# Performance work log

Hardware: AMD Instinct MI355X
Metric: run time of the kernel (lower is better)

The kernel has to match this reference:

```python
import jax, jax.numpy as jnp
import numpy as np

E = 8        # num_experts
C = 1024     # n_emb
H = 4096     # n_emb * ff_mult
B, T = 4, 1024


def setup_inputs() -> dict:
    key = jax.random.key(0)
    k_x, k_g, k_1, k_2, k_3 = jax.random.split(key, 5)
    scale = 0.02
    return {
        "x": jax.random.normal(k_x, (B, T, C), dtype=jnp.float32),
        "Wg": jax.random.normal(k_g, (E, C), dtype=jnp.float32) * scale,   # gate: Linear(C, E), weight [E, C]
        "W1": jax.random.normal(k_1, (E, C, H), dtype=jnp.float32) * scale,  # per-expert w1 (transposed for einsum)
        "W2": jax.random.normal(k_2, (E, H, C), dtype=jnp.float32) * scale,  # per-expert w2
        "W3": jax.random.normal(k_3, (E, C, H), dtype=jnp.float32) * scale,  # per-expert w3
        "top_k": 2,
    }


def reference(x, Wg, W1, W2, W3, top_k):
    Bd, Td, Cd = x.shape
    xf = x.reshape(-1, Cd)                                   # [N, C]
    N = xf.shape[0]
    logits = jnp.einsum('nc,ec->ne', xf, Wg)                 # router logits [N, E]
    probs = jax.nn.softmax(logits.astype(jnp.float32), axis=-1)
    w, sel = jax.lax.top_k(probs, top_k)                     # [N, k]
    w = w / w.sum(axis=-1, keepdims=True)                    # renormalize over selected
    # combine weight per (token, expert): sum of normalized topk weights routed to e
    cw = jnp.zeros((N, E), jnp.float32).at[jnp.arange(N)[:, None], sel].add(w)
    # dense grouped SwiGLU over all experts; combine weights zero out unselected experts
    h1 = jnp.einsum('nc,ech->neh', xf, W1)                   # [N, E, H]
    g = jax.nn.silu(h1) * jnp.einsum('nc,ech->neh', xf, W3)  # [N, E, H]
    out = jnp.einsum('neh,ehc,ne->nc', g, W2, cw.astype(x.dtype))
    return out.reshape(Bd, Td, Cd)
```

## Files before the change

kernel.cpp:

```cpp
#include <hip/hip_runtime.h>
#include <hip/hip_bf16.h>

#define E_     8
#define C_     1024
#define H_     4096
#define N_TOK  4096
#define TOPK   2
#define NSLOT  (N_TOK*TOPK)
#define SPAD   (NSLOT+256)

#define LPAD 40

typedef __attribute__((ext_vector_type(4))) float f32x4;
typedef __attribute__((ext_vector_type(8))) short short8;

__device__ __forceinline__ unsigned short f2bf(float f) {
    return __builtin_bit_cast(unsigned short, __float2bfloat16(f));
}

__device__ __forceinline__ void gload16(const void* g, const void* l) {
    __builtin_amdgcn_global_load_lds(
        (const __attribute__((address_space(1))) unsigned int*)g,
        (__attribute__((address_space(3))) unsigned int*)l, 16, 0, 0);
}

#define WAITVM_(n) asm volatile("s_waitcnt vmcnt(" #n ")" ::: "memory")
#define WAITVM(n) WAITVM_(n)
#define SWZ(r) ((((r)&3) ^ (((r)>>2)&3)))

__global__ void router_kernel(const float* __restrict__ x, const float* __restrict__ Wg,
                              int* __restrict__ sel, float* __restrict__ wts) {
    int wave = (blockIdx.x * blockDim.x + threadIdx.x) >> 6;
    int lane = threadIdx.x & 63;
    if (wave >= N_TOK) return;
    const float* xr = x + (size_t)wave * C_;
    float acc[E_];
#pragma unroll
    for (int e = 0; e < E_; ++e) acc[e] = 0.f;
    for (int c = lane; c < C_; c += 64) {
        float xv = xr[c];
#pragma unroll
        for (int e = 0; e < E_; ++e) acc[e] += xv * Wg[e * C_ + c];
    }
#pragma unroll
    for (int e = 0; e < E_; ++e) {
#pragma unroll
        for (int off = 32; off > 0; off >>= 1) acc[e] += __shfl_xor(acc[e], off);
    }
    if (lane == 0) {
        float mx = acc[0];
#pragma unroll
        for (int e = 1; e < E_; ++e) mx = fmaxf(mx, acc[e]);
        float p[E_]; float s = 0.f;
#pragma unroll
        for (int e = 0; e < E_; ++e) { p[e] = __expf(acc[e] - mx); s += p[e]; }
        float inv = 1.f / s;
#pragma unroll
        for (int e = 0; e < E_; ++e) p[e] *= inv;
        int b0 = 0; float v0 = p[0];
#pragma unroll
        for (int e = 1; e < E_; ++e) if (p[e] > v0) { v0 = p[e]; b0 = e; }
        int b1 = -1; float v1 = -1.f;
#pragma unroll
        for (int e = 0; e < E_; ++e) { if (e != b0 && p[e] > v1) { v1 = p[e]; b1 = e; } }
        float isum = 1.f / (v0 + v1);
        sel[wave*2]   = b0; sel[wave*2+1] = b1;
        wts[wave*2]   = v0 * isum; wts[wave*2+1] = v1 * isum;
    }
}

__global__ void assign_kernel(const int* __restrict__ sel, const float* __restrict__ wts,
                              int* __restrict__ counts, int* __restrict__ offsets,
                              int* __restrict__ pos_of_slot, int* __restrict__ token_of,
                              float* __restrict__ slotw) {
    __shared__ int cnt[256][E_];
    __shared__ int offs[E_];
    int t = threadIdx.x;
    const int PER = NSLOT / 256;
    int base = t * PER;
    int loc[E_];
#pragma unroll
    for (int e = 0; e < E_; ++e) loc[e] = 0;
    for (int i = 0; i < PER; ++i) loc[sel[base + i]]++;
#pragma unroll
    for (int e = 0; e < E_; ++e) cnt[t][e] = loc[e];
    __syncthreads();
    if (t < E_) {
        int run = 0;
        for (int i = 0; i < 256; ++i) { int c = cnt[i][t]; cnt[i][t] = run; run += c; }
        counts[t] = run;
    }
    __syncthreads();
    if (t == 0) {
        int s = 0;
        for (int e = 0; e < E_; ++e) { offs[e] = s; offsets[e] = s; s += counts[e]; }
    }
    __syncthreads();
    int run[E_];
#pragma unroll
    for (int e = 0; e < E_; ++e) run[e] = offs[e] + cnt[t][e];
    for (int i = 0; i < PER; ++i) {
        int s = base + i;
        int e = sel[s];
        int p = run[e]++;
        pos_of_slot[s] = p;
        token_of[p] = s >> 1;
        slotw[p] = wts[s];
    }
}

__global__ void copy_kernel(const float* __restrict__ x, const int* __restrict__ pos_of_slot,
                            unsigned short* __restrict__ Xg) {
    int slot = blockIdx.x * 4 + (threadIdx.x >> 6);
    int lane = threadIdx.x & 63;
    int pos = pos_of_slot[slot];
    int n = slot >> 1;
    const float* xr = x + (size_t)n * C_;
    unsigned short* dst = Xg + (size_t)pos * C_;
#pragma unroll
    for (int i = 0; i < 4; ++i) {
        int c0 = i * 256 + lane * 4;
        float4 v = *(const float4*)(xr + c0);
        ushort4 b;
        b.x = f2bf(v.x); b.y = f2bf(v.y); b.z = f2bf(v.z); b.w = f2bf(v.w);
        *(ushort4*)(dst + c0) = b;
    }
}

__global__ void wconv_kernel(const float* __restrict__ src, unsigned short* __restrict__ dst,
                             int R, int Cc) {
    int e = blockIdx.z;
    int c0 = blockIdx.x * 64;
    int r0 = blockIdx.y * 64;
    const float* s = src + (size_t)e * R * Cc;
    unsigned short* d = dst + (size_t)e * R * Cc;
    __shared__ unsigned short t_[64][72];
    int t = threadIdx.x;
    int tr = t >> 4, tc4 = (t & 15) * 4;
#pragma unroll
    for (int i = 0; i < 4; ++i) {
        int r = tr + i * 16;
        float4 v = *(const float4*)(s + (size_t)(r0 + r) * Cc + c0 + tc4);
        t_[r][tc4+0] = f2bf(v.x); t_[r][tc4+1] = f2bf(v.y);
        t_[r][tc4+2] = f2bf(v.z); t_[r][tc4+3] = f2bf(v.w);
    }
    __syncthreads();
    int oc = t >> 2, seg = (t & 3) * 16;
    short8 w0, w1;
#pragma unroll
    for (int j = 0; j < 8; ++j) {
        w0[j] = (short)t_[seg + j][oc];
        w1[j] = (short)t_[seg + 8 + j][oc];
    }
    unsigned short* dp = d + (size_t)(c0 + oc) * R + r0 + seg;
    *(short8*)dp = w0;
    *(short8*)(dp + 8) = w1;
}


#define G1_NH (C_/32)

__global__ __launch_bounds__(512, 2) void gemm1_ring(
        const unsigned short* __restrict__ Xg, const unsigned short* __restrict__ W1t,
        const unsigned short* __restrict__ W3t, unsigned short* __restrict__ G,
        const int* __restrict__ counts, const int* __restrict__ offsets) {
    int ct = blockIdx.x;
    int rslot = blockIdx.y;
    int e = rslot >> 5, rt = rslot & 31;
    int ne = counts[e];
    if (rt * 256 >= ne) return;
    int row0 = offsets[e] + rt * 256;
    int n0 = ct * 128;

    extern __shared__ char lds[];
    char* As  = lds;
    char* B1s = lds + 65536;
    char* B3s = lds + 98304;

    int tid = threadIdx.x, lane = tid & 63, wid = tid >> 6;
    int wm = wid >> 1, wn = wid & 1;
    int fr = lane & 15, q = lane >> 4;
    int srow = lane >> 2, pchk = lane & 3;

    const unsigned short* Ap  = Xg + (size_t)row0 * C_;
    const unsigned short* B1p = W1t + ((size_t)e * H_ + n0) * C_;
    const unsigned short* B3p = W3t + ((size_t)e * H_ + n0) * C_;

    f32x4 acc1[4][4], acc3[4][4];
#pragma unroll
    for (int m = 0; m < 4; ++m)
#pragma unroll
        for (int n = 0; n < 4; ++n) {
            acc1[m][n] = (f32x4){0.f,0.f,0.f,0.f};
            acc3[m][n] = (f32x4){0.f,0.f,0.f,0.f};
        }

    auto STAGE = [&](int hs, int slot) {
        int k0 = hs * 32;
#pragma unroll
        for (int r = 0; r < 2; ++r) {
            int row = r*128 + wid*16 + srow;
            int sc = pchk ^ SWZ(row);
            gload16(Ap + (size_t)row * C_ + k0 + sc*8,
                    As + slot*16384 + (r*128 + wid*16)*64);
        }
        {
            int row = wid*16 + srow;
            int sc = pchk ^ SWZ(row);
            gload16(B1p + (size_t)row * C_ + k0 + sc*8, B1s + slot*8192 + wid*1024);
            gload16(B3p + (size_t)row * C_ + k0 + sc*8, B3s + slot*8192 + wid*1024);
        }
    };

    STAGE(0, 0); STAGE(1, 1); STAGE(2, 2);
    WAITVM(8);
    __builtin_amdgcn_s_barrier();

    for (int h = 0; h < G1_NH; ++h) {
        int slot = h & 3;
        short8 a[4], b1[4], b3[4];
#pragma unroll
        for (int m = 0; m < 4; ++m) {
            int row = wm*64 + m*16 + fr;
            a[m] = *(const short8*)(As + slot*16384 + row*64 + ((q ^ SWZ(row)) << 4));
        }
#pragma unroll
        for (int n = 0; n < 4; ++n) {
            int row = wn*64 + n*16 + fr;
            int so = row*64 + ((q ^ SWZ(row)) << 4);
            b1[n] = *(const short8*)(B1s + slot*8192 + so);
            b3[n] = *(const short8*)(B3s + slot*8192 + so);
        }
        int hs = (h + 3 < G1_NH) ? h + 3 : G1_NH - 1;
        STAGE(hs, (h + 3) & 3);
        WAITVM(8);
        __builtin_amdgcn_sched_barrier(0);
        __builtin_amdgcn_s_setprio(1);
#pragma unroll
        for (int m = 0; m < 4; ++m)
#pragma unroll
            for (int n = 0; n < 4; ++n) {
                acc1[m][n] = __builtin_amdgcn_mfma_f32_16x16x32_bf16(a[m], b1[n], acc1[m][n], 0, 0, 0);
                acc3[m][n] = __builtin_amdgcn_mfma_f32_16x16x32_bf16(a[m], b3[n], acc3[m][n], 0, 0, 0);
            }
        __builtin_amdgcn_s_setprio(0);
        __builtin_amdgcn_s_barrier();
    }
    WAITVM(0);

#pragma unroll
    for (int m = 0; m < 4; ++m)
#pragma unroll
        for (int rg = 0; rg < 4; ++rg) {
            int row = wm*64 + m*16 + q*4 + rg;
            if (rt * 256 + row < ne) {
                size_t gbase = (size_t)(row0 + row) * H_ + n0 + wn*64;
#pragma unroll
                for (int n = 0; n < 4; ++n) {
                    float h1 = acc1[m][n][rg];
                    float h3 = acc3[m][n][rg];
                    float g = h1 * h3 / (1.f + __expf(-h1));
                    G[gbase + n*16 + fr] = f2bf(g);
                }
            }
        }
}

#define G2_NH (H_/32)

__global__ __launch_bounds__(512, 2) void gemm2_ring(
        const unsigned short* __restrict__ G, const unsigned short* __restrict__ W2t,
        float* __restrict__ out, const int* __restrict__ counts,
        const int* __restrict__ offsets, const int* __restrict__ token_of,
        const float* __restrict__ slotw) {
    int ct = blockIdx.x;
    int rslot = blockIdx.y;
    int e = rslot >> 5, rt = rslot & 31;
    int ne = counts[e];
    if (rt * 256 >= ne) return;
    int row0 = offsets[e] + rt * 256;
    int n0 = ct * 128;

    extern __shared__ char lds[];
    char* As = lds;
    char* Bs = lds + 65536;

    int tid = threadIdx.x, lane = tid & 63, wid = tid >> 6;
    int wm = wid >> 1, wn = wid & 1;
    int fr = lane & 15, q = lane >> 4;
    int srow = lane >> 2, pchk = lane & 3;

    const unsigned short* Ap = G + (size_t)row0 * H_;
    const unsigned short* Bp = W2t + ((size_t)e * C_ + n0) * H_;

    f32x4 acc[4][4];
#pragma unroll
    for (int m = 0; m < 4; ++m)
#pragma unroll
        for (int n = 0; n < 4; ++n) acc[m][n] = (f32x4){0.f,0.f,0.f,0.f};

    auto STAGE = [&](int hs, int slot) {
        int k0 = hs * 32;
#pragma unroll
        for (int r = 0; r < 2; ++r) {
            int row = r*128 + wid*16 + srow;
            int sc = pchk ^ SWZ(row);
            gload16(Ap + (size_t)row * H_ + k0 + sc*8,
                    As + slot*16384 + (r*128 + wid*16)*64);
        }
        {
            int row = wid*16 + srow;
            int sc = pchk ^ SWZ(row);
            gload16(Bp + (size_t)row * H_ + k0 + sc*8, Bs + slot*8192 + wid*1024);
        }
    };

    STAGE(0, 0); STAGE(1, 1); STAGE(2, 2);
    WAITVM(6);
    __builtin_amdgcn_s_barrier();

    for (int h = 0; h < G2_NH; ++h) {
        int slot = h & 3;
        short8 a[4], b[4];
#pragma unroll
        for (int m = 0; m < 4; ++m) {
            int row = wm*64 + m*16 + fr;
            a[m] = *(const short8*)(As + slot*16384 + row*64 + ((q ^ SWZ(row)) << 4));
        }
#pragma unroll
        for (int n = 0; n < 4; ++n) {
            int row = wn*64 + n*16 + fr;
            b[n] = *(const short8*)(Bs + slot*8192 + row*64 + ((q ^ SWZ(row)) << 4));
        }
        int hs = (h + 3 < G2_NH) ? h + 3 : G2_NH - 1;
        STAGE(hs, (h + 3) & 3);
        WAITVM(6);
        __builtin_amdgcn_sched_barrier(0);
        __builtin_amdgcn_s_setprio(1);
#pragma unroll
        for (int m = 0; m < 4; ++m)
#pragma unroll
            for (int n = 0; n < 4; ++n)
                acc[m][n] = __builtin_amdgcn_mfma_f32_16x16x32_bf16(a[m], b[n], acc[m][n], 0, 0, 0);
        __builtin_amdgcn_s_setprio(0);
        __builtin_amdgcn_s_barrier();
    }
    WAITVM(0);

#pragma unroll
    for (int m = 0; m < 4; ++m)
#pragma unroll
        for (int rg = 0; rg < 4; ++rg) {
            int row = wm*64 + m*16 + q*4 + rg;
            if (rt * 256 + row < ne) {
                int grow = row0 + row;
                int tok = token_of[grow];
                float w = slotw[grow];
                float* orow = out + (size_t)tok * C_ + n0 + wn*64;
#pragma unroll
                for (int n = 0; n < 4; ++n)
                    atomicAdd(orow + n*16 + fr, acc[m][n][rg] * w);
            }
        }
}

#define BM 128
#define BN 128
#define BK 32
__global__ __launch_bounds__(256, 2) void gemm1_slow(
        const unsigned short* __restrict__ Xg, const float* __restrict__ W1,
        const float* __restrict__ W3, unsigned short* __restrict__ G,
        const int* __restrict__ counts, const int* __restrict__ offsets) {
    int ct = blockIdx.x;
    int rslot = blockIdx.y;
    int e = rslot >> 5, rt = rslot & 31;
    int ne = counts[e];
    if (rt * BM >= ne) return;
    int row0 = offsets[e] + rt * BM;
    int n0 = ct * BN;

    __shared__ unsigned short As[BM][LPAD];
    __shared__ unsigned short B1s[BN][LPAD];
    __shared__ unsigned short B3s[BN][LPAD];

    int tid = threadIdx.x;
    int lane = tid & 63, wid = tid >> 6;
    int wr = (wid >> 1) * 64, wc = (wid & 1) * 64;

    f32x4 acc1[4][4], acc3[4][4];
#pragma unroll
    for (int m = 0; m < 4; ++m)
#pragma unroll
        for (int n = 0; n < 4; ++n) {
            acc1[m][n] = (f32x4){0.f,0.f,0.f,0.f};
            acc3[m][n] = (f32x4){0.f,0.f,0.f,0.f};
        }

    const float* B1p = W1 + (size_t)e * C_ * H_ + n0;
    const float* B3p = W3 + (size_t)e * C_ * H_ + n0;
    int chunk = tid & 3, rr = tid >> 2;
    int kq = tid >> 5, n4 = tid & 31;

    for (int k0 = 0; k0 < C_; k0 += BK) {
        __syncthreads();
#pragma unroll
        for (int h = 0; h < 2; ++h) {
            int row = rr + h * 64;
            uint4 v = *(const uint4*)(Xg + (size_t)(row0 + row) * C_ + k0 + chunk * 8);
            *(uint4*)&As[row][chunk * 8] = v;
        }
        {
            float4 r0 = *(const float4*)(B1p + (size_t)(k0 + kq*4 + 0) * H_ + n4*4);
            float4 r1 = *(const float4*)(B1p + (size_t)(k0 + kq*4 + 1) * H_ + n4*4);
            float4 r2 = *(const float4*)(B1p + (size_t)(k0 + kq*4 + 2) * H_ + n4*4);
            float4 r3 = *(const float4*)(B1p + (size_t)(k0 + kq*4 + 3) * H_ + n4*4);
            ushort4 w0 = {f2bf(r0.x), f2bf(r1.x), f2bf(r2.x), f2bf(r3.x)};
            ushort4 w1 = {f2bf(r0.y), f2bf(r1.y), f2bf(r2.y), f2bf(r3.y)};
            ushort4 w2 = {f2bf(r0.z), f2bf(r1.z), f2bf(r2.z), f2bf(r3.z)};
            ushort4 w3 = {f2bf(r0.w), f2bf(r1.w), f2bf(r2.w), f2bf(r3.w)};
            *(ushort4*)&B1s[n4*4+0][kq*4] = w0;
            *(ushort4*)&B1s[n4*4+1][kq*4] = w1;
            *(ushort4*)&B1s[n4*4+2][kq*4] = w2;
            *(ushort4*)&B1s[n4*4+3][kq*4] = w3;
            r0 = *(const float4*)(B3p + (size_t)(k0 + kq*4 + 0) * H_ + n4*4);
            r1 = *(const float4*)(B3p + (size_t)(k0 + kq*4 + 1) * H_ + n4*4);
            r2 = *(const float4*)(B3p + (size_t)(k0 + kq*4 + 2) * H_ + n4*4);
            r3 = *(const float4*)(B3p + (size_t)(k0 + kq*4 + 3) * H_ + n4*4);
            w0 = (ushort4){f2bf(r0.x), f2bf(r1.x), f2bf(r2.x), f2bf(r3.x)};
            w1 = (ushort4){f2bf(r0.y), f2bf(r1.y), f2bf(r2.y), f2bf(r3.y)};
            w2 = (ushort4){f2bf(r0.z), f2bf(r1.z), f2bf(r2.z), f2bf(r3.z)};
            w3 = (ushort4){f2bf(r0.w), f2bf(r1.w), f2bf(r2.w), f2bf(r3.w)};
            *(ushort4*)&B3s[n4*4+0][kq*4] = w0;
            *(ushort4*)&B3s[n4*4+1][kq*4] = w1;
            *(ushort4*)&B3s[n4*4+2][kq*4] = w2;
            *(ushort4*)&B3s[n4*4+3][kq*4] = w3;
        }
        __syncthreads();
        int q = lane >> 4, fr = lane & 15;
        short8 a[4], b1[4], b3[4];
#pragma unroll
        for (int m = 0; m < 4; ++m) a[m] = *(const short8*)&As[wr + m*16 + fr][q*8];
#pragma unroll
        for (int n = 0; n < 4; ++n) {
            b1[n] = *(const short8*)&B1s[wc + n*16 + fr][q*8];
            b3[n] = *(const short8*)&B3s[wc + n*16 + fr][q*8];
        }
#pragma unroll
        for (int m = 0; m < 4; ++m)
#pragma unroll
            for (int n = 0; n < 4; ++n) {
                acc1[m][n] = __builtin_amdgcn_mfma_f32_16x16x32_bf16(a[m], b1[n], acc1[m][n], 0, 0, 0);
                acc3[m][n] = __builtin_amdgcn_mfma_f32_16x16x32_bf16(a[m], b3[n], acc3[m][n], 0, 0, 0);
            }
    }
    int q = lane >> 4, cfr = lane & 15;
#pragma unroll
    for (int m = 0; m < 4; ++m) {
#pragma unroll
        for (int rg = 0; rg < 4; ++rg) {
            int row = wr + m*16 + q*4 + rg;
            if (rt * BM + row < ne) {
                size_t gbase = (size_t)(row0 + row) * H_ + n0;
#pragma unroll
                for (int n = 0; n < 4; ++n) {
                    float h1 = acc1[m][n][rg];
                    float h3 = acc3[m][n][rg];
                    float g = h1 * h3 / (1.f + __expf(-h1));
                    G[gbase + wc + n*16 + cfr] = f2bf(g);
                }
            }
        }
    }
}

__global__ __launch_bounds__(256, 2) void gemm2_slow(
        const unsigned short* __restrict__ G, const float* __restrict__ W2,
        float* __restrict__ out, const int* __restrict__ counts,
        const int* __restrict__ offsets, const int* __restrict__ token_of,
        const float* __restrict__ slotw) {
    int ct = blockIdx.x;
    int rslot = blockIdx.y;
    int e = rslot >> 5, rt = rslot & 31;
    int ne = counts[e];
    if (rt * BM >= ne) return;
    int row0 = offsets[e] + rt * BM;
    int n0 = ct * BN;

    __shared__ unsigned short As[BM][LPAD];
    __shared__ unsigned short Bs[BN][LPAD];

    int tid = threadIdx.x;
    int lane = tid & 63, wid = tid >> 6;
    int wr = (wid >> 1) * 64, wc = (wid & 1) * 64;

    f32x4 acc[4][4];
#pragma unroll
    for (int m = 0; m < 4; ++m)
#pragma unroll
        for (int n = 0; n < 4; ++n) acc[m][n] = (f32x4){0.f,0.f,0.f,0.f};

    const float* Bp = W2 + (size_t)e * H_ * C_ + n0;
    int chunk = tid & 3, rr = tid >> 2;
    int kq = tid >> 5, n4 = tid & 31;

    for (int k0 = 0; k0 < H_; k0 += BK) {
        __syncthreads();
#pragma unroll
        for (int h = 0; h < 2; ++h) {
            int row = rr + h * 64;
            uint4 v = *(const uint4*)(G + (size_t)(row0 + row) * H_ + k0 + chunk * 8);
            *(uint4*)&As[row][chunk * 8] = v;
        }
        {
            float4 r0 = *(const float4*)(Bp + (size_t)(k0 + kq*4 + 0) * C_ + n4*4);
            float4 r1 = *(const float4*)(Bp + (size_t)(k0 + kq*4 + 1) * C_ + n4*4);
            float4 r2 = *(const float4*)(Bp + (size_t)(k0 + kq*4 + 2) * C_ + n4*4);
            float4 r3 = *(const float4*)(Bp + (size_t)(k0 + kq*4 + 3) * C_ + n4*4);
            ushort4 w0 = {f2bf(r0.x), f2bf(r1.x), f2bf(r2.x), f2bf(r3.x)};
            ushort4 w1 = {f2bf(r0.y), f2bf(r1.y), f2bf(r2.y), f2bf(r3.y)};
            ushort4 w2 = {f2bf(r0.z), f2bf(r1.z), f2bf(r2.z), f2bf(r3.z)};
            ushort4 w3 = {f2bf(r0.w), f2bf(r1.w), f2bf(r2.w), f2bf(r3.w)};
            *(ushort4*)&Bs[n4*4+0][kq*4] = w0;
            *(ushort4*)&Bs[n4*4+1][kq*4] = w1;
            *(ushort4*)&Bs[n4*4+2][kq*4] = w2;
            *(ushort4*)&Bs[n4*4+3][kq*4] = w3;
        }
        __syncthreads();
        int q = lane >> 4, fr = lane & 15;
        short8 a[4], b[4];
#pragma unroll
        for (int m = 0; m < 4; ++m) a[m] = *(const short8*)&As[wr + m*16 + fr][q*8];
#pragma unroll
        for (int n = 0; n < 4; ++n) b[n] = *(const short8*)&Bs[wc + n*16 + fr][q*8];
#pragma unroll
        for (int m = 0; m < 4; ++m)
#pragma unroll
            for (int n = 0; n < 4; ++n)
                acc[m][n] = __builtin_amdgcn_mfma_f32_16x16x32_bf16(a[m], b[n], acc[m][n], 0, 0, 0);
    }
    int q = lane >> 4, cfr = lane & 15;
#pragma unroll
    for (int m = 0; m < 4; ++m) {
#pragma unroll
        for (int rg = 0; rg < 4; ++rg) {
            int row = wr + m*16 + q*4 + rg;
            if (rt * BM + row < ne) {
                int grow = row0 + row;
                int tok = token_of[grow];
                float w = slotw[grow];
                float* orow = out + (size_t)tok * C_ + n0;
#pragma unroll
                for (int n = 0; n < 4; ++n)
                    atomicAdd(orow + wc + n*16 + cfr, acc[m][n][rg] * w);
            }
        }
    }
}

extern "C" void kernel_launch(void* const* d_in, const int* in_sizes, int n_in,
                              void* d_out, int out_size, void* d_ws, size_t ws_size,
                              hipStream_t stream) {
    const float* x  = (const float*)d_in[0];
    const float* Wg = (const float*)d_in[1];
    const float* W1 = (const float*)d_in[2];
    const float* W2 = (const float*)d_in[3];
    const float* W3 = (const float*)d_in[4];
    float* out = (float*)d_out;

    char* ws = (char*)d_ws;
    size_t o = 0;
    int*   sel      = (int*)(ws + o);  o += (size_t)NSLOT * 4;
    float* wts      = (float*)(ws + o); o += (size_t)NSLOT * 4;
    int*   pos      = (int*)(ws + o);  o += (size_t)NSLOT * 4;
    int*   token_of = (int*)(ws + o);  o += (size_t)NSLOT * 4;
    float* slotw    = (float*)(ws + o); o += (size_t)NSLOT * 4;
    int*   counts   = (int*)(ws + o);
    int*   offsets  = counts + E_;     o += 256;
    unsigned short* Xg = (unsigned short*)(ws + o); o += (size_t)SPAD * C_ * 2;
    unsigned short* G  = (unsigned short*)(ws + o); o += (size_t)SPAD * H_ * 2;
    size_t need_slow = o;
    unsigned short* W1t = (unsigned short*)(ws + o); o += (size_t)E_ * H_ * C_ * 2;
    unsigned short* W3t = (unsigned short*)(ws + o); o += (size_t)E_ * H_ * C_ * 2;
    unsigned short* W2t = W1t;
    size_t need_fast = o;

    hipMemsetAsync(d_out, 0, (size_t)out_size * sizeof(float), stream);
    if (ws_size < need_slow) return;

    router_kernel<<<N_TOK/4, 256, 0, stream>>>(x, Wg, sel, wts);
    assign_kernel<<<1, 256, 0, stream>>>(sel, wts, counts, offsets, pos, token_of, slotw);
    copy_kernel<<<NSLOT/4, 256, 0, stream>>>(x, pos, Xg);

    if (ws_size >= need_fast) {
        hipFuncSetAttribute((const void*)gemm1_ring, hipFuncAttributeMaxDynamicSharedMemorySize, 131072);
        hipFuncSetAttribute((const void*)gemm2_ring, hipFuncAttributeMaxDynamicSharedMemorySize, 98304);
        wconv_kernel<<<dim3(H_/64, C_/64, E_), 256, 0, stream>>>(W1, W1t, C_, H_);
        wconv_kernel<<<dim3(H_/64, C_/64, E_), 256, 0, stream>>>(W3, W3t, C_, H_);
        gemm1_ring<<<dim3(H_/128, E_*32), 512, 131072, stream>>>(Xg, W1t, W3t, G, counts, offsets);
        wconv_kernel<<<dim3(C_/64, H_/64, E_), 256, 0, stream>>>(W2, W2t, H_, C_);
        gemm2_ring<<<dim3(C_/128, E_*32), 512, 98304, stream>>>(G, W2t, out, counts, offsets, token_of, slotw);
    } else {
        gemm1_slow<<<dim3(H_/BN, E_*32), 256, 0, stream>>>(Xg, W1, W3, G, counts, offsets);
        gemm2_slow<<<dim3(C_/BN, E_*32), 256, 0, stream>>>(G, W2, out, counts, offsets, token_of, slotw);
    }
}
```

Baseline: 501.2 us.

## Use fragment-major LDS layout and split gate/up MFMA phases with extra barriers

Replaces the XOR-swizzled row-major LDS tile layout with a fragment-major layout: each lane loads 16 rows by 4 k-chunks and writes them so MFMA operand reads become contiguous 16-byte reads with no swizzle arithmetic. In the gate/up GEMM the main loop is split into two phases, W1 MFMAs then W3 MFMAs, with A staging and B staging interleaved between them and extra workgroup barriers. This is meant to cut LDS bank conflicts and address math and to overlap loads with compute more finely. The cost is extra barriers per iteration and fewer independent MFMAs per phase. Global loads now read 16 rows with strided addresses per wave, which may coalesce less well.

```diff
diff --git a/kernel.cpp b/kernel.cpp
--- a/kernel.cpp
+++ b/kernel.cpp
@@ -26,7 +26,6 @@
 
 #define WAITVM_(n) asm volatile("s_waitcnt vmcnt(" #n ")" ::: "memory")
 #define WAITVM(n) WAITVM_(n)
-#define SWZ(r) ((((r)&3) ^ (((r)>>2)&3)))
 
 __global__ void router_kernel(const float* __restrict__ x, const float* __restrict__ Wg,
                               int* __restrict__ sel, float* __restrict__ wts) {
@@ -180,7 +179,7 @@
     int tid = threadIdx.x, lane = tid & 63, wid = tid >> 6;
     int wm = wid >> 1, wn = wid & 1;
     int fr = lane & 15, q = lane >> 4;
-    int srow = lane >> 2, pchk = lane & 3;
+    int arow = lane & 15, akch = lane >> 4;
 
     const unsigned short* Ap  = Xg + (size_t)row0 * C_;
     const unsigned short* B1p = W1t + ((size_t)e * H_ + n0) * C_;
@@ -195,54 +194,64 @@
             acc3[m][n] = (f32x4){0.f,0.f,0.f,0.f};
         }
 
-    auto STAGE = [&](int hs, int slot) {
+    auto STAGE_A = [&](int hs, int slot) {
         int k0 = hs * 32;
 #pragma unroll
-        for (int r = 0; r < 2; ++r) {
-            int row = r*128 + wid*16 + srow;
-            int sc = pchk ^ SWZ(row);
-            gload16(Ap + (size_t)row * C_ + k0 + sc*8,
-                    As + slot*16384 + (r*128 + wid*16)*64);
-        }
-        {
-            int row = wid*16 + srow;
-            int sc = pchk ^ SWZ(row);
-            gload16(B1p + (size_t)row * C_ + k0 + sc*8, B1s + slot*8192 + wid*1024);
-            gload16(B3p + (size_t)row * C_ + k0 + sc*8, B3s + slot*8192 + wid*1024);
+        for (int j = 0; j < 2; ++j) {
+            int g = wid + j * 8;
+            gload16(Ap + (size_t)(g * 16 + arow) * C_ + k0 + akch * 8,
+                    As + slot * 16384 + g * 1024);
         }
     };
-
-    STAGE(0, 0); STAGE(1, 1); STAGE(2, 2);
+    auto STAGE_B = [&](int hs, int slot) {
+        int k0 = hs * 32;
+        gload16(B1p + (size_t)(wid * 16 + arow) * C_ + k0 + akch * 8,
+                B1s + slot * 8192 + wid * 1024);
+        gload16(B3p + (size_t)(wid * 16 + arow) * C_ + k0 + akch * 8,
+                B3s + slot * 8192 + wid * 1024);
+    };
+
+    STAGE_A(0, 0); STAGE_B(0, 0);
+    STAGE_A(1, 1); STAGE_B(1, 1);
+    STAGE_A(2, 2); STAGE_B(2, 2);
     WAITVM(8);
     __builtin_amdgcn_s_barrier();
 
     for (int h = 0; h < G1_NH; ++h) {
         int slot = h & 3;
+        int hs = (h + 3 < G1_NH) ? h + 3 : G1_NH - 1;
+        int wslot = (h + 3) & 3;
         short8 a[4], b1[4], b3[4];
 #pragma unroll
-        for (int m = 0; m < 4; ++m) {
-            int row = wm*64 + m*16 + fr;
-            a[m] = *(const short8*)(As + slot*16384 + row*64 + ((q ^ SWZ(row)) << 4));
-        }
-#pragma unroll
-        for (int n = 0; n < 4; ++n) {
-            int row = wn*64 + n*16 + fr;
-            int so = row*64 + ((q ^ SWZ(row)) << 4);
-            b1[n] = *(const short8*)(B1s + slot*8192 + so);
-            b3[n] = *(const short8*)(B3s + slot*8192 + so);
-        }
-        int hs = (h + 3 < G1_NH) ? h + 3 : G1_NH - 1;
-        STAGE(hs, (h + 3) & 3);
+        for (int m = 0; m < 4; ++m)
+            a[m] = *(const short8*)(As + slot * 16384 + (wm * 4 + m) * 1024 + q * 256 + fr * 16);
+#pragma unroll
+        for (int n = 0; n < 4; ++n)
+            b1[n] = *(const short8*)(B1s + slot * 8192 + (wn * 4 + n) * 1024 + q * 256 + fr * 16);
+        STAGE_A(hs, wslot);
+        __builtin_amdgcn_sched_barrier(0);
+        __builtin_amdgcn_s_barrier();
+        __builtin_amdgcn_s_setprio(1);
+#pragma unroll
+        for (int m = 0; m < 4; ++m)
+#pragma unroll
+            for (int n = 0; n < 4; ++n)
+                acc1[m][n] = __builtin_amdgcn_mfma_f32_16x16x32_bf16(a[m], b1[n], acc1[m][n], 0, 0, 0);
+        __builtin_amdgcn_s_setprio(0);
+        __builtin_amdgcn_s_barrier();
+#pragma unroll
+        for (int n = 0; n < 4; ++n)
+            b3[n] = *(const short8*)(B3s + slot * 8192 + (wn * 4 + n) * 1024 + q * 256 + fr * 16);
+        STAGE_B(hs, wslot);
         WAITVM(8);
         __builtin_amdgcn_sched_barrier(0);
+        __builtin_amdgcn_s_barrier();
         __builtin_amdgcn_s_setprio(1);
 #pragma unroll
         for (int m = 0; m < 4; ++m)
 #pragma unroll
-            for (int n = 0; n < 4; ++n) {
-                acc1[m][n] = __builtin_amdgcn_mfma_f32_16x16x32_bf16(a[m], b1[n], acc1[m][n], 0, 0, 0);
+            for (int n = 0; n < 4; ++n)
                 acc3[m][n] = __builtin_amdgcn_mfma_f32_16x16x32_bf16(a[m], b3[n], acc3[m][n], 0, 0, 0);
-            }
         __builtin_amdgcn_s_setprio(0);
         __builtin_amdgcn_s_barrier();
     }
@@ -288,7 +297,7 @@
     int tid = threadIdx.x, lane = tid & 63, wid = tid >> 6;
     int wm = wid >> 1, wn = wid & 1;
     int fr = lane & 15, q = lane >> 4;
-    int srow = lane >> 2, pchk = lane & 3;
+    int arow = lane & 15, akch = lane >> 4;
 
     const unsigned short* Ap = G + (size_t)row0 * H_;
     const unsigned short* Bp = W2t + ((size_t)e * C_ + n0) * H_;
@@ -302,17 +311,13 @@
     auto STAGE = [&](int hs, int slot) {
         int k0 = hs * 32;
 #pragma unroll
-        for (int r = 0; r < 2; ++r) {
-            int row = r*128 + wid*16 + srow;
-            int sc = pchk ^ SWZ(row);
-            gload16(Ap + (size_t)row * H_ + k0 + sc*8,
-                    As + slot*16384 + (r*128 + wid*16)*64);
-        }
-        {
-            int row = wid*16 + srow;
-            int sc = pchk ^ SWZ(row);
-            gload16(Bp + (size_t)row * H_ + k0 + sc*8, Bs + slot*8192 + wid*1024);
-        }
+        for (int j = 0; j < 2; ++j) {
+            int g = wid + j * 8;
+            gload16(Ap + (size_t)(g * 16 + arow) * H_ + k0 + akch * 8,
+                    As + slot * 16384 + g * 1024);
+        }
+        gload16(Bp + (size_t)(wid * 16 + arow) * H_ + k0 + akch * 8,
+                Bs + slot * 8192 + wid * 1024);
     };
 
     STAGE(0, 0); STAGE(1, 1); STAGE(2, 2);
@@ -321,21 +326,18 @@
 
     for (int h = 0; h < G2_NH; ++h) {
         int slot = h & 3;
+        int hs = (h + 3 < G2_NH) ? h + 3 : G2_NH - 1;
         short8 a[4], b[4];
 #pragma unroll
-        for (int m = 0; m < 4; ++m) {
-            int row = wm*64 + m*16 + fr;
-            a[m] = *(const short8*)(As + slot*16384 + row*64 + ((q ^ SWZ(row)) << 4));
-        }
-#pragma unroll
-        for (int n = 0; n < 4; ++n) {
-            int row = wn*64 + n*16 + fr;
-            b[n] = *(const short8*)(Bs + slot*8192 + row*64 + ((q ^ SWZ(row)) << 4));
-        }
-        int hs = (h + 3 < G2_NH) ? h + 3 : G2_NH - 1;
+        for (int m = 0; m < 4; ++m)
+            a[m] = *(const short8*)(As + slot * 16384 + (wm * 4 + m) * 1024 + q * 256 + fr * 16);
+#pragma unroll
+        for (int n = 0; n < 4; ++n)
+            b[n] = *(const short8*)(Bs + slot * 8192 + (wn * 4 + n) * 1024 + q * 256 + fr * 16);
         STAGE(hs, (h + 3) & 3);
         WAITVM(6);
         __builtin_amdgcn_sched_barrier(0);
+        __builtin_amdgcn_s_barrier();
         __builtin_amdgcn_s_setprio(1);
 #pragma unroll
         for (int m = 0; m < 4; ++m)
```

Result: slower. 590.4 us (+17.8%).

## Use 256x256 GEMM tiles with interleaved W1/W3 layout and split-K GEMM2

Applied to the files above, without the earlier changes.

The W1 and W3 weights are converted into one interleaved bf16 buffer, so GEMM1 runs a single 256x256 tile that yields paired h1/h3 columns for the SwiGLU epilogue. Both GEMMs switch from a 4-slot ring with K=32 steps to a double-buffered K=64 pipeline. It has four phases per step, issuing half-tile loads between barrier-separated MFMA groups and using an 8-row-group LDS layout. GEMM2 now uses 256-wide output tiles and a 4-way split of the H reduction across blocks, which raises parallelism and reuse but quadruples the atomic adds into the output. The larger tiles and more barriers per step may lower occupancy, and the layout drops the earlier XOR swizzle, which could introduce LDS bank conflicts.

```diff
diff --git a/kernel.cpp b/kernel.cpp
--- a/kernel.cpp
+++ b/kernel.cpp
@@ -26,7 +26,6 @@
 
 #define WAITVM_(n) asm volatile("s_waitcnt vmcnt(" #n ")" ::: "memory")
 #define WAITVM(n) WAITVM_(n)
-#define SWZ(r) ((((r)&3) ^ (((r)>>2)&3)))
 
 __global__ void router_kernel(const float* __restrict__ x, const float* __restrict__ Wg,
                               int* __restrict__ sel, float* __restrict__ wts) {
@@ -157,12 +156,44 @@
     *(short8*)(dp + 8) = w1;
 }
 
-
-#define G1_NH (C_/32)
-
-__global__ __launch_bounds__(512, 2) void gemm1_ring(
-        const unsigned short* __restrict__ Xg, const unsigned short* __restrict__ W1t,
-        const unsigned short* __restrict__ W3t, unsigned short* __restrict__ G,
+__global__ void wconv13_kernel(const float* __restrict__ src, unsigned short* __restrict__ dst,
+                               int is3) {
+    int e = blockIdx.z;
+    int c0 = blockIdx.x * 64;
+    int r0 = blockIdx.y * 64;
+    const float* s = src + (size_t)e * C_ * H_;
+    unsigned short* d = dst + (size_t)e * 8192 * C_;
+    __shared__ unsigned short t_[64][72];
+    int t = threadIdx.x;
+    int tr = t >> 4, tc4 = (t & 15) * 4;
+#pragma unroll
+    for (int i = 0; i < 4; ++i) {
+        int r = tr + i * 16;
+        float4 v = *(const float4*)(s + (size_t)(r0 + r) * H_ + c0 + tc4);
+        t_[r][tc4+0] = f2bf(v.x); t_[r][tc4+1] = f2bf(v.y);
+        t_[r][tc4+2] = f2bf(v.z); t_[r][tc4+3] = f2bf(v.w);
+    }
+    __syncthreads();
+    int oc = t >> 2, seg = (t & 3) * 16;
+    short8 w0, w1;
+#pragma unroll
+    for (int j = 0; j < 8; ++j) {
+        w0[j] = (short)t_[seg + j][oc];
+        w1[j] = (short)t_[seg + 8 + j][oc];
+    }
+    int h = c0 + oc;
+    int nI = ((h >> 4) << 5) + (h & 15) + is3 * 16;
+    unsigned short* dp = d + (size_t)nI * C_ + r0 + seg;
+    *(short8*)dp = w0;
+    *(short8*)(dp + 8) = w1;
+}
+
+
+#define LDSOFF(lr, kc) ((((lr) >> 3) << 10) + ((kc) << 7) + (((lr) & 7) << 4))
+
+__global__ __launch_bounds__(512, 2) void gemm1_256(
+        const unsigned short* __restrict__ Xg, const unsigned short* __restrict__ W13t,
+        unsigned short* __restrict__ G,
         const int* __restrict__ counts, const int* __restrict__ offsets) {
     int ct = blockIdx.x;
     int rslot = blockIdx.y;
@@ -170,196 +201,194 @@
     int ne = counts[e];
     if (rt * 256 >= ne) return;
     int row0 = offsets[e] + rt * 256;
-    int n0 = ct * 128;
 
     extern __shared__ char lds[];
-    char* As  = lds;
-    char* B1s = lds + 65536;
-    char* B3s = lds + 98304;
 
     int tid = threadIdx.x, lane = tid & 63, wid = tid >> 6;
-    int wm = wid >> 1, wn = wid & 1;
+    int wm = wid >> 2, wn = wid & 3;
     int fr = lane & 15, q = lane >> 4;
-    int srow = lane >> 2, pchk = lane & 3;
-
-    const unsigned short* Ap  = Xg + (size_t)row0 * C_;
-    const unsigned short* B1p = W1t + ((size_t)e * H_ + n0) * C_;
-    const unsigned short* B3p = W3t + ((size_t)e * H_ + n0) * C_;
-
-    f32x4 acc1[4][4], acc3[4][4];
-#pragma unroll
-    for (int m = 0; m < 4; ++m)
-#pragma unroll
-        for (int n = 0; n < 4; ++n) {
-            acc1[m][n] = (f32x4){0.f,0.f,0.f,0.f};
-            acc3[m][n] = (f32x4){0.f,0.f,0.f,0.f};
-        }
-
-    auto STAGE = [&](int hs, int slot) {
-        int k0 = hs * 32;
-#pragma unroll
-        for (int r = 0; r < 2; ++r) {
-            int row = r*128 + wid*16 + srow;
-            int sc = pchk ^ SWZ(row);
-            gload16(Ap + (size_t)row * C_ + k0 + sc*8,
-                    As + slot*16384 + (r*128 + wid*16)*64);
-        }
-        {
-            int row = wid*16 + srow;
-            int sc = pchk ^ SWZ(row);
-            gload16(B1p + (size_t)row * C_ + k0 + sc*8, B1s + slot*8192 + wid*1024);
-            gload16(B3p + (size_t)row * C_ + k0 + sc*8, B3s + slot*8192 + wid*1024);
+    int sr = lane & 7, sc = lane >> 3;
+
+    const unsigned short* Ap = Xg + (size_t)row0 * C_;
+    const unsigned short* Bp = W13t + ((size_t)e * 8192 + ct * 256) * C_;
+
+    f32x4 acc[8][4];
+#pragma unroll
+    for (int m = 0; m < 8; ++m)
+#pragma unroll
+        for (int n = 0; n < 4; ++n) acc[m][n] = (f32x4){0.f,0.f,0.f,0.f};
+
+    auto STAGE_A = [&](int ts, int half, int dd) {
+        int k0 = ts * 64;
+#pragma unroll
+        for (int j = 0; j < 2; ++j) {
+            int g = wid * 2 + j;
+            int row = half * 128 + g * 8 + sr;
+            gload16(Ap + (size_t)row * C_ + k0 + sc * 8,
+                    lds + dd * 65536 + half * 16384 + g * 1024);
         }
     };
-
-    STAGE(0, 0); STAGE(1, 1); STAGE(2, 2);
-    WAITVM(8);
-    __builtin_amdgcn_s_barrier();
-
-    for (int h = 0; h < G1_NH; ++h) {
-        int slot = h & 3;
-        short8 a[4], b1[4], b3[4];
-#pragma unroll
-        for (int m = 0; m < 4; ++m) {
-            int row = wm*64 + m*16 + fr;
-            a[m] = *(const short8*)(As + slot*16384 + row*64 + ((q ^ SWZ(row)) << 4));
-        }
-#pragma unroll
-        for (int n = 0; n < 4; ++n) {
-            int row = wn*64 + n*16 + fr;
-            int so = row*64 + ((q ^ SWZ(row)) << 4);
-            b1[n] = *(const short8*)(B1s + slot*8192 + so);
-            b3[n] = *(const short8*)(B3s + slot*8192 + so);
-        }
-        int hs = (h + 3 < G1_NH) ? h + 3 : G1_NH - 1;
-        STAGE(hs, (h + 3) & 3);
-        WAITVM(8);
-        __builtin_amdgcn_sched_barrier(0);
-        __builtin_amdgcn_s_setprio(1);
-#pragma unroll
-        for (int m = 0; m < 4; ++m)
-#pragma unroll
-            for (int n = 0; n < 4; ++n) {
-                acc1[m][n] = __builtin_amdgcn_mfma_f32_16x16x32_bf16(a[m], b1[n], acc1[m][n], 0, 0, 0);
-                acc3[m][n] = __builtin_amdgcn_mfma_f32_16x16x32_bf16(a[m], b3[n], acc3[m][n], 0, 0, 0);
-            }
-        __builtin_amdgcn_s_setprio(0);
-        __builtin_amdgcn_s_barrier();
+    auto STAGE_B = [&](int ts, int half, int dd) {
+        int k0 = ts * 64;
+#pragma unroll
+        for (int j = 0; j < 2; ++j) {
+            int g = wid * 2 + j;
+            int row = half * 128 + g * 8 + sr;
+            gload16(Bp + (size_t)row * C_ + k0 + sc * 8,
+                    lds + dd * 65536 + 32768 + half * 16384 + g * 1024);
+        }
+    };
+
+    STAGE_A(0, 0, 0); STAGE_A(0, 1, 0); STAGE_B(0, 0, 0); STAGE_B(0, 1, 0);
+
+    const int NT = C_ / 64;
+    short8 af[4], bf_[4];
+    for (int t = 0; t < NT; ++t) {
+        int d = t & 1, dn = d ^ 1;
+        int ts = (t + 1 < NT) ? t + 1 : t;
+        const char* Abase = lds + d * 65536 + wm * 16384;
+        const char* Bbase = lds + d * 65536 + 32768 + (wn >> 1) * 16384;
+
+#define G1_PH(STG, WN, KS, MH, RDB)                                                  \
+        __builtin_amdgcn_s_barrier();                                                \
+        STG;                                                                         \
+        WAITVM(WN);                                                                  \
+        __builtin_amdgcn_s_barrier();                                                \
+        __builtin_amdgcn_sched_barrier(0);                                           \
+        {                                                                            \
+            int kc = (KS) * 4 + q;                                                   \
+            _Pragma("unroll")                                                        \
+            for (int m = 0; m < 4; ++m) {                                            \
+                int lr = ((MH) * 4 + m) * 16 + fr;                                   \
+                af[m] = *(const short8*)(Abase + LDSOFF(lr, kc));                    \
+            }                                                                        \
+            if (RDB) {                                                               \
+                _Pragma("unroll")                                                    \
+                for (int n = 0; n < 4; ++n) {                                        \
+                    int lrb = (wn & 1) * 64 + n * 16 + fr;                           \
+                    bf_[n] = *(const short8*)(Bbase + LDSOFF(lrb, kc));              \
+                }                                                                    \
+            }                                                                        \
+            __builtin_amdgcn_s_setprio(1);                                           \
+            _Pragma("unroll")                                                        \
+            for (int m = 0; m < 4; ++m)                                              \
+                _Pragma("unroll")                                                    \
+                for (int n = 0; n < 4; ++n)                                          \
+                    acc[(MH)*4 + m][n] = __builtin_amdgcn_mfma_f32_16x16x32_bf16(    \
+                        af[m], bf_[n], acc[(MH)*4 + m][n], 0, 0, 0);                 \
+            __builtin_amdgcn_s_setprio(0);                                           \
+        }
+
+        G1_PH(STAGE_A(ts, 0, dn), 2, 0, 0, 1)
+        G1_PH(STAGE_A(ts, 1, dn), 4, 0, 1, 0)
+        G1_PH(STAGE_B(ts, 0, dn), 6, 1, 0, 1)
+        G1_PH(STAGE_B(ts, 1, dn), 8, 1, 1, 0)
     }
     WAITVM(0);
 
 #pragma unroll
-    for (int m = 0; m < 4; ++m)
+    for (int m = 0; m < 8; ++m)
 #pragma unroll
         for (int rg = 0; rg < 4; ++rg) {
-            int row = wm*64 + m*16 + q*4 + rg;
+            int row = wm * 128 + m * 16 + q * 4 + rg;
             if (rt * 256 + row < ne) {
-                size_t gbase = (size_t)(row0 + row) * H_ + n0 + wn*64;
-#pragma unroll
-                for (int n = 0; n < 4; ++n) {
-                    float h1 = acc1[m][n][rg];
-                    float h3 = acc3[m][n][rg];
+                size_t gbase = (size_t)(row0 + row) * H_;
+#pragma unroll
+                for (int pi = 0; pi < 2; ++pi) {
+                    float h1 = acc[m][2 * pi][rg];
+                    float h3 = acc[m][2 * pi + 1][rg];
                     float g = h1 * h3 / (1.f + __expf(-h1));
-                    G[gbase + n*16 + fr] = f2bf(g);
+                    int h = (ct * 8 + wn * 2 + pi) * 16 + fr;
+                    G[gbase + h] = f2bf(g);
                 }
             }
         }
 }
 
-#define G2_NH (H_/32)
-
-__global__ __launch_bounds__(512, 2) void gemm2_ring(
+__global__ __launch_bounds__(512, 2) void gemm2_256(
         const unsigned short* __restrict__ G, const unsigned short* __restrict__ W2t,
         float* __restrict__ out, const int* __restrict__ counts,
         const int* __restrict__ offsets, const int* __restrict__ token_of,
         const float* __restrict__ slotw) {
-    int ct = blockIdx.x;
-    int rslot = blockIdx.y;
-    int e = rslot >> 5, rt = rslot & 31;
+    int b = blockIdx.x;
+    int e = b & 7;
+    int j = b >> 3;
+    int ksp = j & 3;
+    int ct = (j >> 2) & 3;
+    int rt = j >> 4;
     int ne = counts[e];
     if (rt * 256 >= ne) return;
     int row0 = offsets[e] + rt * 256;
-    int n0 = ct * 128;
+    int n0 = ct * 256;
+    int kbase = ksp * (H_ / 4);
 
     extern __shared__ char lds[];
-    char* As = lds;
-    char* Bs = lds + 65536;
 
     int tid = threadIdx.x, lane = tid & 63, wid = tid >> 6;
-    int wm = wid >> 1, wn = wid & 1;
+    int wm = wid >> 2, wn = wid & 3;
     int fr = lane & 15, q = lane >> 4;
-    int srow = lane >> 2, pchk = lane & 3;
-
-    const unsigned short* Ap = G + (size_t)row0 * H_;
-    const unsigned short* Bp = W2t + ((size_t)e * C_ + n0) * H_;
-
-    f32x4 acc[4][4];
-#pragma unroll
-    for (int m = 0; m < 4; ++m)
+    int sr = lane & 7, sc = lane >> 3;
+
+    const unsigned short* Ap = G + (size_t)row0 * H_ + kbase;
+    const unsigned short* Bp = W2t + ((size_t)e * C_ + n0) * H_ + kbase;
+
+    f32x4 acc[8][4];
+#pragma unroll
+    for (int m = 0; m < 8; ++m)
 #pragma unroll
         for (int n = 0; n < 4; ++n) acc[m][n] = (f32x4){0.f,0.f,0.f,0.f};
 
-    auto STAGE = [&](int hs, int slot) {
-        int k0 = hs * 32;
-#pragma unroll
-        for (int r = 0; r < 2; ++r) {
-            int row = r*128 + wid*16 + srow;
-            int sc = pchk ^ SWZ(row);
-            gload16(Ap + (size_t)row * H_ + k0 + sc*8,
-                    As + slot*16384 + (r*128 + wid*16)*64);
-        }
-        {
-            int row = wid*16 + srow;
-            int sc = pchk ^ SWZ(row);
-            gload16(Bp + (size_t)row * H_ + k0 + sc*8, Bs + slot*8192 + wid*1024);
+    auto STAGE_A = [&](int ts, int half, int dd) {
+        int k0 = ts * 64;
+#pragma unroll
+        for (int j2 = 0; j2 < 2; ++j2) {
+            int g = wid * 2 + j2;
+            int row = half * 128 + g * 8 + sr;
+            gload16(Ap + (size_t)row * H_ + k0 + sc * 8,
+                    lds + dd * 65536 + half * 16384 + g * 1024);
         }
     };
-
-    STAGE(0, 0); STAGE(1, 1); STAGE(2, 2);
-    WAITVM(6);
-    __builtin_amdgcn_s_barrier();
-
-    for (int h = 0; h < G2_NH; ++h) {
-        int slot = h & 3;
-        short8 a[4], b[4];
-#pragma unroll
-        for (int m = 0; m < 4; ++m) {
-            int row = wm*64 + m*16 + fr;
-            a[m] = *(const short8*)(As + slot*16384 + row*64 + ((q ^ SWZ(row)) << 4));
-        }
-#pragma unroll
-        for (int n = 0; n < 4; ++n) {
-            int row = wn*64 + n*16 + fr;
-            b[n] = *(const short8*)(Bs + slot*8192 + row*64 + ((q ^ SWZ(row)) << 4));
-        }
-        int hs = (h + 3 < G2_NH) ? h + 3 : G2_NH - 1;
-        STAGE(hs, (h + 3) & 3);
-        WAITVM(6);
-        __builtin_amdgcn_sched_barrier(0);
-        __builtin_amdgcn_s_setprio(1);
-#pragma unroll
-        for (int m = 0; m < 4; ++m)
-#pragma unroll
-            for (int n = 0; n < 4; ++n)
-                acc[m][n] = __builtin_amdgcn_mfma_f32_16x16x32_bf16(a[m], b[n], acc[m][n], 0, 0, 0);
-        __builtin_amdgcn_s_setprio(0);
-        __builtin_amdgcn_s_barrier();
+    auto STAGE_B = [&](int ts, int half, int dd) {
+        int k0 = ts * 64;
+#pragma unroll
+        for (int j2 = 0; j2 < 2; ++j2) {
+            int g = wid * 2 + j2;
+            int row = half * 128 + g * 8 + sr;
+            gload16(Bp + (size_t)row * H_ + k0 + sc * 8,
+                    lds + dd * 65536 + 32768 + half * 16384 + g * 1024);
+        }
+    };
+
+    STAGE_A(0, 0, 0); STAGE_A(0, 1, 0); STAGE_B(0, 0, 0); STAGE_B(0, 1, 0);
+
+    const int NT = (H_ / 4) / 64;
+    short8 af[4], bf_[4];
+    for (int t = 0; t < NT; ++t) {
+        int d = t & 1, dn = d ^ 1;
+        int ts = (t + 1 < NT) ? t + 1 : t;
+        const char* Abase = lds + d * 65536 + wm * 16384;
+        const char* Bbase = lds + d * 65536 + 32768 + (wn >> 1) * 16384;
+
+        G1_PH(STAGE_A(ts, 0, dn), 2, 0, 0, 1)
+        G1_PH(STAGE_A(ts, 1, dn), 4, 0, 1, 0)
+        G1_PH(STAGE_B(ts, 0, dn), 6, 1, 0, 1)
+        G1_PH(STAGE_B(ts, 1, dn), 8, 1, 1, 0)
     }
     WAITVM(0);
 
 #pragma unroll
-    for (int m = 0; m < 4; ++m)
+    for (int m = 0; m < 8; ++m)
 #pragma unroll
         for (int rg = 0; rg < 4; ++rg) {
-            int row = wm*64 + m*16 + q*4 + rg;
+            int row = wm * 128 + m * 16 + q * 4 + rg;
             if (rt * 256 + row < ne) {
                 int grow = row0 + row;
                 int tok = token_of[grow];
                 float w = slotw[grow];
-                float* orow = out + (size_t)tok * C_ + n0 + wn*64;
+                float* orow = out + (size_t)tok * C_ + n0 + wn * 64;
 #pragma unroll
                 for (int n = 0; n < 4; ++n)
-                    atomicAdd(orow + n*16 + fr, acc[m][n][rg] * w);
+                    atomicAdd(orow + n * 16 + fr, acc[m][n][rg] * w);
             }
         }
 }
@@ -579,9 +608,8 @@
     unsigned short* Xg = (unsigned short*)(ws + o); o += (size_t)SPAD * C_ * 2;
     unsigned short* G  = (unsigned short*)(ws + o); o += (size_t)SPAD * H_ * 2;
     size_t need_slow = o;
-    unsigned short* W1t = (unsigned short*)(ws + o); o += (size_t)E_ * H_ * C_ * 2;
-    unsigned short* W3t = (unsigned short*)(ws + o); o += (size_t)E_ * H_ * C_ * 2;
-    unsigned short* W2t = W1t;
+    unsigned short* W13t = (unsigned short*)(ws + o); o += (size_t)E_ * 8192 * C_ * 2;
+    unsigned short* W2t  = W13t;
     size_t need_fast = o;
 
     hipMemsetAsync(d_out, 0, (size_t)out_size * sizeof(float), stream);
@@ -592,13 +620,13 @@
     copy_kernel<<<NSLOT/4, 256, 0, stream>>>(x, pos, Xg);
 
     if (ws_size >= need_fast) {
-        hipFuncSetAttribute((const void*)gemm1_ring, hipFuncAttributeMaxDynamicSharedMemorySize, 131072);
-        hipFuncSetAttribute((const void*)gemm2_ring, hipFuncAttributeMaxDynamicSharedMemorySize, 98304);
-        wconv_kernel<<<dim3(H_/64, C_/64, E_), 256, 0, stream>>>(W1, W1t, C_, H_);
-        wconv_kernel<<<dim3(H_/64, C_/64, E_), 256, 0, stream>>>(W3, W3t, C_, H_);
-        gemm1_ring<<<dim3(H_/128, E_*32), 512, 131072, stream>>>(Xg, W1t, W3t, G, counts, offsets);
+        hipFuncSetAttribute((const void*)gemm1_256, hipFuncAttributeMaxDynamicSharedMemorySize, 131072);
+        hipFuncSetAttribute((const void*)gemm2_256, hipFuncAttributeMaxDynamicSharedMemorySize, 131072);
+        wconv13_kernel<<<dim3(H_/64, C_/64, E_), 256, 0, stream>>>(W1, W13t, 0);
+        wconv13_kernel<<<dim3(H_/64, C_/64, E_), 256, 0, stream>>>(W3, W13t, 1);
+        gemm1_256<<<dim3(32, 256), 512, 131072, stream>>>(Xg, W13t, G, counts, offsets);
         wconv_kernel<<<dim3(C_/64, H_/64, E_), 256, 0, stream>>>(W2, W2t, H_, C_);
-        gemm2_ring<<<dim3(C_/128, E_*32), 512, 98304, stream>>>(G, W2t, out, counts, offsets, token_of, slotw);
+        gemm2_256<<<4096, 512, 131072, stream>>>(G, W2t, out, counts, offsets, token_of, slotw);
     } else {
         gemm1_slow<<<dim3(H_/BN, E_*32), 256, 0, stream>>>(Xg, W1, W3, G, counts, offsets);
         gemm2_slow<<<dim3(C_/BN, E_*32), 256, 0, stream>>>(G, W2, out, counts, offsets, token_of, slotw);
```

Measured after the change: 586.7 us. 1.17x slower.
